# Optimization experiments

Hardware: AMD Instinct MI355X
Metric: run time of the kernel (lower is better)

## Reference

```python
import jax, jax.numpy as jnp
import numpy as np

NEG_INF = -1e9

def setup_inputs() -> dict:
    key = jax.random.key(0)
    ks = jax.random.split(key, 6)
    B, M, RNN, H, D = 64, 1024, 1024, 512, 2048
    return {
        "h": jax.random.normal(ks[0], (B, RNN), dtype=jnp.float32),
        "att_feats": jax.random.normal(ks[1], (B, M, D), dtype=jnp.float32),
        "att_mask": jax.random.randint(ks[2], (B, M), 0, 2, dtype=jnp.int32),
        "p_att_feats": jax.random.normal(ks[3], (B, M, H), dtype=jnp.float32),
        "W_ah": jax.random.normal(ks[4], (H, RNN), dtype=jnp.float32) * (1.0 / np.sqrt(RNN)),
        "w_alpha": jax.random.normal(ks[5], (H,), dtype=jnp.float32) * (1.0 / np.sqrt(H)),
    }

def reference(h, att_feats, att_mask, p_att_feats, W_ah, w_alpha):
    # Wah(h): [B, H]
    wah = h @ W_ah.T
    # additive attention energies: tanh(Wah(h)[:, None, :] + p_att_feats) -> [B, M, H]
    e = jnp.tanh(wah[:, None, :] + p_att_feats)
    # project to scalar per region: [B, M]
    logits = jnp.einsum("bmh,h->bm", e, w_alpha)
    logits = jnp.where(att_mask == 0, NEG_INF, logits)
    alpha = jax.nn.softmax(logits, axis=-1)
    # weighted sum of region features: [B, D]
    att = jnp.einsum("bm,bmd->bd", alpha, att_feats)
    return att
```

## Files before the change

### kernel.cpp

```cpp
#include <hip/hip_runtime.h>
#include <math.h>

#define B   64
#define M   1024
#define RNN 1024
#define H   512
#define D   2048

#define NCHUNK 16
#define CROWS  (M / NCHUNK)
#define RPW    (CROWS / 4)

__device__ __forceinline__ float fast_tanh(float x) {
    float ax = fabsf(x);
    float t  = __expf(-2.0f * ax);
    float r  = (1.0f - t) * __builtin_amdgcn_rcpf(1.0f + t);
    return copysignf(r, x);
}

__global__ __launch_bounds__(256) void k_wah(const float* __restrict__ h,
                                             const float* __restrict__ W,
                                             float* __restrict__ wah) {
    int wid  = (blockIdx.x * 256 + threadIdx.x) >> 6;
    int lane = threadIdx.x & 63;
    int b = wid >> 9;
    int j = wid & (H - 1);
    const float4* hp = (const float4*)(h + (size_t)b * RNN);
    const float4* wp = (const float4*)(W + (size_t)j * RNN);
    float acc = 0.0f;
#pragma unroll
    for (int t = 0; t < 4; ++t) {
        int i = lane + t * 64;
        float4 a = hp[i];
        float4 w = wp[i];
        acc += a.x * w.x + a.y * w.y + a.z * w.z + a.w * w.w;
    }
#pragma unroll
    for (int off = 32; off > 0; off >>= 1)
        acc += __shfl_down(acc, off);
    if (lane == 0) wah[wid] = acc;
}

__global__ __launch_bounds__(256) void k_fused(const float* __restrict__ wah,
                                               const float* __restrict__ p_att,
                                               const int* __restrict__ mask,
                                               const float* __restrict__ w_alpha,
                                               const float* __restrict__ feats,
                                               float* __restrict__ partial,
                                               float* __restrict__ zpart) {
    const int b   = blockIdx.x;
    const int c   = blockIdx.y;
    const int tid = threadIdx.x;
    const int lane = tid & 63;
    const int w    = tid >> 6;

    __shared__ float          s_w[CROWS];
    __shared__ float          s_zred[4];
    __shared__ unsigned short s_idx[CROWS + 4];
    __shared__ float          s_val[CROWS + 4];
    __shared__ int            s_cnt;

    const float4* wh4 = (const float4*)(wah + (size_t)b * H);
    const float4* wa4 = (const float4*)w_alpha;
    float4 wh0 = wh4[lane], wh1 = wh4[lane + 64];
    float4 wa0 = wa4[lane], wa1 = wa4[lane + 64];

    const int   m0   = c * CROWS;
    const int*  mrow = mask + (size_t)b * M + m0;
    const float4* pb4 = (const float4*)(p_att + ((size_t)b * M + m0) * H);

    float zsum = 0.0f;
    for (int r = w * RPW; r < w * RPW + RPW; ++r) {
        float e = 0.0f;
        if (mrow[r] != 0) {
            float4 p0 = pb4[(size_t)r * (H / 4) + lane];
            float4 p1 = pb4[(size_t)r * (H / 4) + 64 + lane];
            float s = fast_tanh(p0.x + wh0.x) * wa0.x
                    + fast_tanh(p0.y + wh0.y) * wa0.y
                    + fast_tanh(p0.z + wh0.z) * wa0.z
                    + fast_tanh(p0.w + wh0.w) * wa0.w
                    + fast_tanh(p1.x + wh1.x) * wa1.x
                    + fast_tanh(p1.y + wh1.y) * wa1.y
                    + fast_tanh(p1.z + wh1.z) * wa1.z
                    + fast_tanh(p1.w + wh1.w) * wa1.w;
#pragma unroll
            for (int off = 32; off > 0; off >>= 1)
                s += __shfl_xor(s, off);
            e = __expf(s);
        }
        if (lane == 0) s_w[r] = e;
        zsum += e;
    }
    if (lane == 0) s_zred[w] = zsum;
    __syncthreads();
    if (tid == 0)
        zpart[(size_t)c * B + b] = (s_zred[0] + s_zred[1]) + (s_zred[2] + s_zred[3]);

    if (tid < CROWS) {
        float a = s_w[tid];
        bool pred = (a != 0.0f);
        unsigned long long bal = __ballot(pred);
        int pos = __popcll(bal & ((1ull << lane) - 1ull));
        if (pred) { s_idx[pos] = (unsigned short)tid; s_val[pos] = a; }
        int cnt  = __popcll(bal);
        int npad = (cnt + 3) & ~3;
        if (lane < npad - cnt) { s_idx[cnt + lane] = 0; s_val[cnt + lane] = 0.0f; }
        if (lane == 0) s_cnt = npad;
    }
    __syncthreads();
    const int n = s_cnt;

    const float4* fb4 = (const float4*)(feats + ((size_t)b * M + m0) * D)
                        + (size_t)w * 128 + lane;
    float4 acc0 = {0.f, 0.f, 0.f, 0.f}, acc1 = {0.f, 0.f, 0.f, 0.f};
    for (int i = 0; i < n; i += 4) {
        int   r0 = s_idx[i],     r1 = s_idx[i + 1];
        int   r2 = s_idx[i + 2], r3 = s_idx[i + 3];
        float v0 = s_val[i],     v1 = s_val[i + 1];
        float v2 = s_val[i + 2], v3 = s_val[i + 3];
        const float4* q0 = fb4 + (size_t)r0 * (D / 4);
        const float4* q1 = fb4 + (size_t)r1 * (D / 4);
        const float4* q2 = fb4 + (size_t)r2 * (D / 4);
        const float4* q3 = fb4 + (size_t)r3 * (D / 4);
        float4 f00 = q0[0], f01 = q0[64];
        float4 f10 = q1[0], f11 = q1[64];
        float4 f20 = q2[0], f21 = q2[64];
        float4 f30 = q3[0], f31 = q3[64];
        acc0.x += v0 * f00.x; acc0.y += v0 * f00.y; acc0.z += v0 * f00.z; acc0.w += v0 * f00.w;
        acc1.x += v0 * f01.x; acc1.y += v0 * f01.y; acc1.z += v0 * f01.z; acc1.w += v0 * f01.w;
        acc0.x += v1 * f10.x; acc0.y += v1 * f10.y; acc0.z += v1 * f10.z; acc0.w += v1 * f10.w;
        acc1.x += v1 * f11.x; acc1.y += v1 * f11.y; acc1.z += v1 * f11.z; acc1.w += v1 * f11.w;
        acc0.x += v2 * f20.x; acc0.y += v2 * f20.y; acc0.z += v2 * f20.z; acc0.w += v2 * f20.w;
        acc1.x += v2 * f21.x; acc1.y += v2 * f21.y; acc1.z += v2 * f21.z; acc1.w += v2 * f21.w;
        acc0.x += v3 * f30.x; acc0.y += v3 * f30.y; acc0.z += v3 * f30.z; acc0.w += v3 * f30.w;
        acc1.x += v3 * f31.x; acc1.y += v3 * f31.y; acc1.z += v3 * f31.z; acc1.w += v3 * f31.w;
    }
    float4* ob = (float4*)(partial + ((size_t)c * B + b) * D) + (size_t)w * 128 + lane;
    ob[0]  = acc0;
    ob[64] = acc1;
}

__global__ __launch_bounds__(256) void k_reduce(const float* __restrict__ partial,
                                                const float* __restrict__ zpart,
                                                float* __restrict__ out) {
    int i4 = blockIdx.x * 256 + threadIdx.x;
    int b  = i4 >> 9;
    float Z = 0.0f;
#pragma unroll
    for (int c = 0; c < NCHUNK; ++c)
        Z += zpart[c * B + b];
    const float4* p4 = (const float4*)partial;
    float4 s = p4[i4];
#pragma unroll
    for (int c = 1; c < NCHUNK; ++c) {
        float4 v = p4[(size_t)c * (B * D / 4) + i4];
        s.x += v.x; s.y += v.y; s.z += v.z; s.w += v.w;
    }
    float inv = 1.0f / Z;
    float4 r = {s.x * inv, s.y * inv, s.z * inv, s.w * inv};
    ((float4*)out)[i4] = r;
}

extern "C" void kernel_launch(void* const* d_in, const int* in_sizes, int n_in,
                              void* d_out, int out_size, void* d_ws, size_t ws_size,
                              hipStream_t stream) {
    const float* h       = (const float*)d_in[0];
    const float* feats   = (const float*)d_in[1];
    const int*   mask    = (const int*)d_in[2];
    const float* p_att   = (const float*)d_in[3];
    const float* W_ah    = (const float*)d_in[4];
    const float* w_alpha = (const float*)d_in[5];
    float* out = (float*)d_out;

    float* ws      = (float*)d_ws;
    float* wah     = ws;
    float* zpart   = wah + B * H;
    float* partial = zpart + NCHUNK * B;

    k_wah   <<<dim3(B * H / 4), 256, 0, stream>>>(h, W_ah, wah);
    k_fused <<<dim3(B, NCHUNK), 256, 0, stream>>>(wah, p_att, mask, w_alpha, feats,
                                                  partial, zpart);
    k_reduce<<<dim3(B * D / 1024), 256, 0, stream>>>(partial, zpart, out);
}
```

Measured before the change: 80.52 us.

## Fuse final reduction into attention kernel via ticket counter; tile Wah GEMV

The separate reduce kernel is removed. Instead, the last chunk block for each batch row, found with an atomic ticket counter and thread fences, sums the partial results and normalises them in place. The Wah projection kernel is restructured so each block stages 16 rows of h in shared memory and reuses W rows held in registers across 16 batch entries, and it also clears the tickets. Padding entries now repeat the last valid row index rather than row 0. This saves one kernel launch and reduces redundant global loads of h and W, at the cost of atomics, fences and a serial tail of reduction work inside the last block per batch row.

```diff
diff --git a/kernel.cpp b/kernel.cpp
--- a/kernel.cpp
+++ b/kernel.cpp
@@ -20,25 +20,45 @@
 
 __global__ __launch_bounds__(256) void k_wah(const float* __restrict__ h,
                                              const float* __restrict__ W,
-                                             float* __restrict__ wah) {
-    int wid  = (blockIdx.x * 256 + threadIdx.x) >> 6;
-    int lane = threadIdx.x & 63;
-    int b = wid >> 9;
-    int j = wid & (H - 1);
-    const float4* hp = (const float4*)(h + (size_t)b * RNN);
-    const float4* wp = (const float4*)(W + (size_t)j * RNN);
-    float acc = 0.0f;
-#pragma unroll
-    for (int t = 0; t < 4; ++t) {
-        int i = lane + t * 64;
-        float4 a = hp[i];
-        float4 w = wp[i];
-        acc += a.x * w.x + a.y * w.y + a.z * w.z + a.w * w.w;
-    }
-#pragma unroll
-    for (int off = 32; off > 0; off >>= 1)
-        acc += __shfl_down(acc, off);
-    if (lane == 0) wah[wid] = acc;
+                                             float* __restrict__ wah,
+                                             int* __restrict__ tickets) {
+    if (blockIdx.x == 0 && blockIdx.y == 0 && threadIdx.x < B)
+        tickets[threadIdx.x] = 0;
+
+    const int tid = threadIdx.x, lane = tid & 63, w = tid >> 6;
+    const int bt = blockIdx.y * 16;
+    const int j0 = blockIdx.x * 8 + w * 2;
+
+    __shared__ float s_h[16 * RNN];
+    const float4* h4  = (const float4*)(h + (size_t)bt * RNN);
+    float4*       sh4 = (float4*)s_h;
+#pragma unroll
+    for (int k = 0; k < 16; ++k)
+        sh4[tid + k * 256] = h4[tid + k * 256];
+
+    const float4* Wa = (const float4*)(W + (size_t)j0 * RNN);
+    const float4* Wb = (const float4*)(W + (size_t)(j0 + 1) * RNN);
+    float4 wa[4], wb[4];
+#pragma unroll
+    for (int k = 0; k < 4; ++k) { wa[k] = Wa[lane + 64 * k]; wb[k] = Wb[lane + 64 * k]; }
+    __syncthreads();
+
+    for (int b = 0; b < 16; ++b) {
+        float d0 = 0.0f, d1 = 0.0f;
+#pragma unroll
+        for (int k = 0; k < 4; ++k) {
+            float4 hv = sh4[b * 256 + lane + 64 * k];
+            d0 += hv.x * wa[k].x + hv.y * wa[k].y + hv.z * wa[k].z + hv.w * wa[k].w;
+            d1 += hv.x * wb[k].x + hv.y * wb[k].y + hv.z * wb[k].z + hv.w * wb[k].w;
+        }
+#pragma unroll
+        for (int off = 32; off > 0; off >>= 1) {
+            d0 += __shfl_xor(d0, off);
+            d1 += __shfl_xor(d1, off);
+        }
+        if (lane == 0)
+            *(float2*)(wah + (size_t)(bt + b) * H + j0) = make_float2(d0, d1);
+    }
 }
 
 __global__ __launch_bounds__(256) void k_fused(const float* __restrict__ wah,
@@ -47,7 +67,9 @@
                                                const float* __restrict__ w_alpha,
                                                const float* __restrict__ feats,
                                                float* __restrict__ partial,
-                                               float* __restrict__ zpart) {
+                                               float* __restrict__ zpart,
+                                               int* __restrict__ tickets,
+                                               float* __restrict__ out) {
     const int b   = blockIdx.x;
     const int c   = blockIdx.y;
     const int tid = threadIdx.x;
@@ -58,16 +80,17 @@
     __shared__ float          s_zred[4];
     __shared__ unsigned short s_idx[CROWS + 4];
     __shared__ float          s_val[CROWS + 4];
-    __shared__ int            s_cnt;
+    __shared__ int            s_cntreal;
+    __shared__ int            s_ticket;
 
     const float4* wh4 = (const float4*)(wah + (size_t)b * H);
     const float4* wa4 = (const float4*)w_alpha;
     float4 wh0 = wh4[lane], wh1 = wh4[lane + 64];
     float4 wa0 = wa4[lane], wa1 = wa4[lane + 64];
 
-    const int   m0   = c * CROWS;
-    const int*  mrow = mask + (size_t)b * M + m0;
-    const float4* pb4 = (const float4*)(p_att + ((size_t)b * M + m0) * H);
+    const int     m0   = c * CROWS;
+    const int*    mrow = mask + (size_t)b * M + m0;
+    const float4* pb4  = (const float4*)(p_att + ((size_t)b * M + m0) * H);
 
     float zsum = 0.0f;
     for (int r = w * RPW; r < w * RPW + RPW; ++r) {
@@ -102,13 +125,16 @@
         unsigned long long bal = __ballot(pred);
         int pos = __popcll(bal & ((1ull << lane) - 1ull));
         if (pred) { s_idx[pos] = (unsigned short)tid; s_val[pos] = a; }
-        int cnt  = __popcll(bal);
-        int npad = (cnt + 3) & ~3;
-        if (lane < npad - cnt) { s_idx[cnt + lane] = 0; s_val[cnt + lane] = 0.0f; }
-        if (lane == 0) s_cnt = npad;
-    }
-    __syncthreads();
-    const int n = s_cnt;
+        if (lane == 0) s_cntreal = __popcll(bal);
+    }
+    __syncthreads();
+    const int cnt = s_cntreal;
+    const int n   = (cnt + 3) & ~3;
+    if (tid >= cnt && tid < n) {
+        s_idx[tid] = (cnt > 0) ? s_idx[cnt - 1] : (unsigned short)0;
+        s_val[tid] = 0.0f;
+    }
+    __syncthreads();
 
     const float4* fb4 = (const float4*)(feats + ((size_t)b * M + m0) * D)
                         + (size_t)w * 128 + lane;
@@ -138,27 +164,31 @@
     float4* ob = (float4*)(partial + ((size_t)c * B + b) * D) + (size_t)w * 128 + lane;
     ob[0]  = acc0;
     ob[64] = acc1;
-}
-
-__global__ __launch_bounds__(256) void k_reduce(const float* __restrict__ partial,
-                                                const float* __restrict__ zpart,
-                                                float* __restrict__ out) {
-    int i4 = blockIdx.x * 256 + threadIdx.x;
-    int b  = i4 >> 9;
+
+    __threadfence();
+    if (tid == 0) s_ticket = atomicAdd(&tickets[b], 1);
+    __syncthreads();
+    if (s_ticket != NCHUNK - 1) return;
+    __threadfence();
+
     float Z = 0.0f;
 #pragma unroll
-    for (int c = 0; c < NCHUNK; ++c)
-        Z += zpart[c * B + b];
+    for (int c2 = 0; c2 < NCHUNK; ++c2)
+        Z += zpart[(size_t)c2 * B + b];
+    const float invZ = 1.0f / Z;
+
     const float4* p4 = (const float4*)partial;
-    float4 s = p4[i4];
-#pragma unroll
-    for (int c = 1; c < NCHUNK; ++c) {
-        float4 v = p4[(size_t)c * (B * D / 4) + i4];
-        s.x += v.x; s.y += v.y; s.z += v.z; s.w += v.w;
-    }
-    float inv = 1.0f / Z;
-    float4 r = {s.x * inv, s.y * inv, s.z * inv, s.w * inv};
-    ((float4*)out)[i4] = r;
+#pragma unroll
+    for (int t = tid; t < D / 4; t += 256) {
+        float4 s = {0.f, 0.f, 0.f, 0.f};
+#pragma unroll
+        for (int c2 = 0; c2 < NCHUNK; ++c2) {
+            float4 v = p4[((size_t)c2 * B + b) * (D / 4) + t];
+            s.x += v.x; s.y += v.y; s.z += v.z; s.w += v.w;
+        }
+        float4 r = {s.x * invZ, s.y * invZ, s.z * invZ, s.w * invZ};
+        ((float4*)out)[(size_t)b * (D / 4) + t] = r;
+    }
 }
 
 extern "C" void kernel_launch(void* const* d_in, const int* in_sizes, int n_in,
@@ -176,9 +206,9 @@
     float* wah     = ws;
     float* zpart   = wah + B * H;
     float* partial = zpart + NCHUNK * B;
-
-    k_wah   <<<dim3(B * H / 4), 256, 0, stream>>>(h, W_ah, wah);
-    k_fused <<<dim3(B, NCHUNK), 256, 0, stream>>>(wah, p_att, mask, w_alpha, feats,
-                                                  partial, zpart);
-    k_reduce<<<dim3(B * D / 1024), 256, 0, stream>>>(partial, zpart, out);
-}
+    int*   tickets = (int*)(partial + (size_t)NCHUNK * B * D);
+
+    k_wah  <<<dim3(H / 8, B / 16), 256, 0, stream>>>(h, W_ah, wah, tickets);
+    k_fused<<<dim3(B, NCHUNK), 256, 0, stream>>>(wah, p_att, mask, w_alpha, feats,
+                                                 partial, zpart, tickets, out);
+}
```

Result: slower. 277.8 us (+245.1%).
